# Performance work log

Measured on AMD Instinct MI355X. Metric: run time of the kernel, lower is better.

## Reference

```python
import jax, jax.numpy as jnp
import numpy as np

H = 16  # num_heads

def setup_inputs() -> dict:
    key = jax.random.key(0)
    ks = jax.random.split(key, 6)
    B, T, C, S = 2, 2048, 1024, 2048
    return {
        "q": jax.random.normal(ks[0], (B, T, C), jnp.float32),
        "k_xl": jax.random.normal(ks[1], (B, S, C), jnp.float32),
        "v_xl": jax.random.normal(ks[2], (B, S, C), jnp.float32),
        "W_qkv": jax.random.normal(ks[3], (3 * C, C), jnp.float32) * (1.0 / np.sqrt(C)),
        "W_proj": jax.random.normal(ks[4], (C, C), jnp.float32) * (1.0 / np.sqrt(C)),
        "pos_emb": jax.random.normal(ks[5], (S, C), jnp.float32),
        "is_causal": 0,
    }

def reference(q, k_xl, v_xl, W_qkv, W_proj, pos_emb, is_causal):
    B, T, C = q.shape
    hd = C // H
    # self_attention: W_qkv(q).split(d_model, -1)
    qkv = jnp.einsum('btc,dc->btd', q, W_qkv)  # [B,T,3C]
    qn, kn, vn = jnp.split(qkv, 3, axis=-1)
    # XL cache gets positional embedding added before use
    kx = k_xl + pos_emb[None, :, :]            # [B,S,C]
    vx = v_xl

    def to_heads(x):
        b, s, c = x.shape
        return x.reshape(b, s, H, hd).transpose(0, 2, 1, 3)  # [B,H,s,hd]

    qh = to_heads(qn)
    kcat = jnp.concatenate([to_heads(kx), to_heads(kn)], axis=2)  # [B,H,S+T,hd]
    vcat = jnp.concatenate([to_heads(vx), to_heads(vn)], axis=2)
    scale = 1.0 / jnp.sqrt(jnp.asarray(hd, qh.dtype))
    scores = jnp.einsum('bhtd,bhsd->bhts', qh, kcat) * scale  # [B,H,T,S+T]
    attn = jax.nn.softmax(scores, axis=-1)
    y = jnp.einsum('bhts,bhsd->bhtd', attn, vcat)  # [B,H,T,hd]
    y = y.transpose(0, 2, 1, 3).reshape(B, T, C)
    return jnp.einsum('btc,dc->btd', y, W_proj)
```

## Files before the change

kernel.cpp:

```cpp
#include <hip/hip_runtime.h>

typedef unsigned short u16;
typedef unsigned int u32;
typedef u16 u16x4 __attribute__((ext_vector_type(4)));
typedef u16 u16x8 __attribute__((ext_vector_type(8)));
typedef __bf16 bf16x8 __attribute__((ext_vector_type(8)));
typedef float f32x4 __attribute__((ext_vector_type(4)));
typedef float f32x16 __attribute__((ext_vector_type(16)));

static __device__ __forceinline__ u16 f2bf(float f) {
  union { float f; u32 u; } x; x.f = f;
  u32 r = x.u + 0x7fffu + ((x.u >> 16) & 1u);
  return (u16)(r >> 16);
}
static __device__ __forceinline__ u32 packbf(float a, float b) {
  union { u32 u; __bf16 h[2]; } x; x.h[0] = (__bf16)a; x.h[1] = (__bf16)b; return x.u;
}
static __device__ __forceinline__ void pl32swap(u32& a, u32& b) {
  asm volatile("v_permlane32_swap_b32 %0, %1" : "+v"(a), "+v"(b));
}
static __device__ __forceinline__ void gload16(const void* g, void* l) {
  __builtin_amdgcn_global_load_lds((const __attribute__((address_space(1))) unsigned int*)g,
                                   (__attribute__((address_space(3))) unsigned int*)l, 16, 0, 0);
}

__global__ __launch_bounds__(256) void cvt_all(const float* __restrict__ q, const float* __restrict__ wqkv_f,
                                               const float* __restrict__ wproj_f, u16* __restrict__ qbf,
                                               u16* __restrict__ wqkv, u16* __restrict__ wproj, float sc) {
  int i = blockIdx.x * 256 + threadIdx.x;
  const float* src;
  u16* dst;
  int j;
  float s = 1.0f;
  if (i < 1048576) { src = q; dst = qbf; j = i; }
  else if (i < 1835008) { j = i - 1048576; src = wqkv_f; dst = wqkv; if (j < 262144) s = sc; }
  else { j = i - 1835008; src = wproj_f; dst = wproj; }
  float4 v = reinterpret_cast<const float4*>(src)[j];
  u16x4 o; o[0] = f2bf(v.x * s); o[1] = f2bf(v.y * s); o[2] = f2bf(v.z * s); o[3] = f2bf(v.w * s);
  reinterpret_cast<u16x4*>(dst)[j] = o;
}

template <int OUT_BF16>
__global__ __launch_bounds__(256, 2) void gemm_bt2(const u16* __restrict__ A, const u16* __restrict__ B,
                                                   void* __restrict__ Cout, int M, int N, int K) {
  __shared__ alignas(128) u16 As[8192];
  __shared__ alignas(128) u16 Bs[8192];
  const int tid = threadIdx.x;
  const int m0 = blockIdx.y * 128, n0 = blockIdx.x * 128;
  const int wid = tid >> 6, lane = tid & 63;
  const int lm = lane & 15, lg = lane >> 4;
  const int wm = (wid >> 1) * 64, wn = (wid & 1) * 64;
  int srow[4], scol[4];
#pragma unroll
  for (int i = 0; i < 4; i++) {
    int li = tid + i * 256;
    srow[i] = li >> 3;
    scol[i] = ((li & 7) ^ (srow[i] & 7)) * 8;
  }
  f32x4 acc[4][4] = {};
  for (int k0 = 0; k0 < K; k0 += 64) {
    __syncthreads();
#pragma unroll
    for (int i = 0; i < 4; i++) {
      gload16(&A[(size_t)(m0 + srow[i]) * K + k0 + scol[i]], &As[(size_t)(i * 256 + wid * 64) * 8]);
      gload16(&B[(size_t)(n0 + srow[i]) * K + k0 + scol[i]], &Bs[(size_t)(i * 256 + wid * 64) * 8]);
    }
    __syncthreads();
#pragma unroll
    for (int ks = 0; ks < 2; ks++) {
      bf16x8 af[4], bfr[4];
#pragma unroll
      for (int mi = 0; mi < 4; mi++) {
        int row = wm + mi * 16 + lm;
        af[mi] = *(const bf16x8*)&As[row * 64 + (((ks * 4 + lg) ^ (row & 7)) << 3)];
      }
#pragma unroll
      for (int ni = 0; ni < 4; ni++) {
        int row = wn + ni * 16 + lm;
        bfr[ni] = *(const bf16x8*)&Bs[row * 64 + (((ks * 4 + lg) ^ (row & 7)) << 3)];
      }
#pragma unroll
      for (int mi = 0; mi < 4; mi++)
#pragma unroll
        for (int ni = 0; ni < 4; ni++)
          acc[mi][ni] = __builtin_amdgcn_mfma_f32_16x16x32_bf16(af[mi], bfr[ni], acc[mi][ni], 0, 0, 0);
    }
  }
#pragma unroll
  for (int mi = 0; mi < 4; mi++)
#pragma unroll
    for (int ni = 0; ni < 4; ni++)
#pragma unroll
      for (int r = 0; r < 4; r++) {
        int row = m0 + wm + mi * 16 + lg * 4 + r;
        int col = n0 + wn + ni * 16 + lm;
        if (OUT_BF16) ((u16*)Cout)[(size_t)row * N + col] = f2bf(acc[mi][ni][r]);
        else          ((float*)Cout)[(size_t)row * N + col] = acc[mi][ni][r];
      }
}

__global__ __launch_bounds__(256) void build_kxl(const float* __restrict__ k_xl, const float* __restrict__ pos,
                                                 u16* __restrict__ khxl) {
  int idx = blockIdx.x * 256 + threadIdx.x;
  int d8 = idx & 7;
  int s = (idx >> 3) & 2047;
  int bh = idx >> 14;
  int b = bh >> 4, h = bh & 15;
  size_t src = ((size_t)(b * 2048 + s)) * 1024 + h * 64 + d8 * 8;
  size_t ps = ((size_t)s) * 1024 + h * 64 + d8 * 8;
  float4 a0 = *(const float4*)&k_xl[src];
  float4 a1 = *(const float4*)&k_xl[src + 4];
  float4 p0 = *(const float4*)&pos[ps];
  float4 p1 = *(const float4*)&pos[ps + 4];
  u16x8 o;
  o[0] = f2bf(a0.x + p0.x); o[1] = f2bf(a0.y + p0.y); o[2] = f2bf(a0.z + p0.z); o[3] = f2bf(a0.w + p0.w);
  o[4] = f2bf(a1.x + p1.x); o[5] = f2bf(a1.y + p1.y); o[6] = f2bf(a1.z + p1.z); o[7] = f2bf(a1.w + p1.w);
  *(u16x8*)&khxl[((size_t)bh * 2048 + s) * 64 + d8 * 8] = o;
}

__global__ __launch_bounds__(256) void build_vt(const float* __restrict__ v_xl, const u16* __restrict__ qkvb,
                                                u16* __restrict__ Vt) {
  __shared__ u16 tile[64][72];
  const int bh = blockIdx.y, b = bh >> 4, h = bh & 15;
  const int s0 = blockIdx.x * 64;
  const int tid = threadIdx.x;
  {
    int sl = tid >> 2;
    int dseg = (tid & 3) * 16;
    if (s0 < 2048) {
      const float* src = v_xl + ((size_t)(b * 2048 + s0 + sl)) * 1024 + h * 64 + dseg;
#pragma unroll
      for (int j = 0; j < 16; j += 4) {
        float4 v = *(const float4*)&src[j];
        tile[sl][dseg + j] = f2bf(v.x);
        tile[sl][dseg + j + 1] = f2bf(v.y);
        tile[sl][dseg + j + 2] = f2bf(v.z);
        tile[sl][dseg + j + 3] = f2bf(v.w);
      }
    } else {
      const u16* src = qkvb + ((size_t)(b * 2048 + s0 - 2048 + sl)) * 3072 + 2048 + h * 64 + dseg;
      *(u16x8*)&tile[sl][dseg] = *(const u16x8*)&src[0];
      *(u16x8*)&tile[sl][dseg + 8] = *(const u16x8*)&src[8];
    }
  }
  __syncthreads();
  {
    int d = tid >> 2;
    int sseg = (tid & 3) * 16;
    u16* dst = Vt + ((size_t)bh * 64 + d) * 4096 + s0 + sseg;
    u16x8 o0, o1;
#pragma unroll
    for (int j = 0; j < 8; j++) { o0[j] = tile[sseg + j][d]; o1[j] = tile[sseg + 8 + j][d]; }
    *(u16x8*)&dst[0] = o0;
    *(u16x8*)&dst[8] = o1;
  }
}

__global__ __launch_bounds__(256, 4) void attn_fwd5(const u16* __restrict__ qkvb, const u16* __restrict__ khxl,
                                                    const u16* __restrict__ vt, u16* __restrict__ Y) {
  const int T = 2048;
  __shared__ alignas(128) u16 KsF[2][4096];
  __shared__ alignas(128) u16 VsF[2][4096];
  const int bh = blockIdx.y;
  const int q0 = blockIdx.x * 64;
  const int tid = threadIdx.x, wid = tid >> 6, lane = tid & 63;
  const int qt = wid & 1, ks = wid >> 1;
  const int l31 = lane & 31, hi = lane >> 5;
  const int sw = l31 & 7;
  const int b = bh >> 4, h = bh & 15;
  const int q = q0 + qt * 32 + l31;
  const u16* Qp = qkvb + (size_t)(b * T + q) * 3072 + h * 64;
  bf16x8 qf[4];
#pragma unroll
  for (int c = 0; c < 4; c++) qf[c] = *(const bf16x8*)&Qp[c * 16 + hi * 8];
  const u16* kxl_p[2];
  const u16* knew_p[2];
  const u16* v_p[2];
  int dsto[2];
#pragma unroll
  for (int i = 0; i < 2; i++) {
    int li = tid + i * 256;
    int srow = li >> 3, scol = ((li & 7) ^ (srow & 7)) * 8;
    kxl_p[i] = khxl + (size_t)bh * 2048 * 64 + (size_t)srow * 64 + scol;
    knew_p[i] = qkvb + (size_t)(b * T + srow) * 3072 + 1024 + h * 64 + scol;
    v_p[i] = vt + ((size_t)bh * 64 + srow) * 4096 + scol;
    dsto[i] = (i * 256 + wid * 64) * 8;
  }
  f32x16 accA = {0.0f}, accB = {0.0f};
  float lrun = 0.0f;
#pragma unroll
  for (int i = 0; i < 2; i++) {
    gload16(kxl_p[i], &KsF[0][dsto[i]]);
    gload16(v_p[i], &VsF[0][dsto[i]]);
  }
  int cur = 0;
  const int krow = ks * 32 + l31;
  for (int t = 0; t < 64; ++t) {
    __syncthreads();
    if (t + 1 < 64) {
      const int nt = t + 1;
#pragma unroll
      for (int i = 0; i < 2; i++) {
        const u16* ksrc = (nt < 32) ? kxl_p[i] + (size_t)nt * 4096
                                    : knew_p[i] + (size_t)(nt - 32) * 196608;
        gload16(ksrc, &KsF[cur ^ 1][dsto[i]]);
        gload16(v_p[i] + nt * 64, &VsF[cur ^ 1][dsto[i]]);
      }
    }
    const u16* Ksb = KsF[cur];
    const u16* Vsb = VsF[cur];
    f32x16 s = {0.0f};
    __builtin_amdgcn_s_setprio(1);
#pragma unroll
    for (int c = 0; c < 4; c++) {
      int cg = 2 * c + hi;
      bf16x8 kf = *(const bf16x8*)&Ksb[krow * 64 + ((cg ^ sw) << 3)];
      s = __builtin_amdgcn_mfma_f32_32x32x16_bf16(kf, qf[c], s, 0, 0, 0);
    }
    __builtin_amdgcn_s_setprio(0);
#pragma unroll
    for (int r = 0; r < 16; r++) s[r] = __builtin_amdgcn_exp2f(s[r]);
    float r0 = ((s[0] + s[1]) + (s[2] + s[3])) + ((s[4] + s[5]) + (s[6] + s[7]));
    float r1 = ((s[8] + s[9]) + (s[10] + s[11])) + ((s[12] + s[13]) + (s[14] + s[15]));
    lrun += r0 + r1;
    u32 w[4][2];
#pragma unroll
    for (int g = 0; g < 4; g++) {
      w[g][0] = packbf(s[4 * g + 0], s[4 * g + 1]);
      w[g][1] = packbf(s[4 * g + 2], s[4 * g + 3]);
    }
    __builtin_amdgcn_s_setprio(1);
#pragma unroll
    for (int m2 = 0; m2 < 2; m2++) {
      int m = ks * 2 + m2;
      u32 W0 = w[2 * m2][0], W2 = w[2 * m2 + 1][0];
      pl32swap(W0, W2);
      u32 W1 = w[2 * m2][1], W3 = w[2 * m2 + 1][1];
      pl32swap(W1, W3);
      union { u32 u[4]; bf16x8 v; } pf;
      pf.u[0] = W0; pf.u[1] = W1; pf.u[2] = W2; pf.u[3] = W3;
      int cg = 2 * m + hi;
      bf16x8 v0 = *(const bf16x8*)&Vsb[l31 * 64 + ((cg ^ sw) << 3)];
      bf16x8 v1 = *(const bf16x8*)&Vsb[(32 + l31) * 64 + ((cg ^ sw) << 3)];
      accA = __builtin_amdgcn_mfma_f32_32x32x16_bf16(v0, pf.v, accA, 0, 0, 0);
      accB = __builtin_amdgcn_mfma_f32_32x32x16_bf16(v1, pf.v, accB, 0, 0, 0);
    }
    __builtin_amdgcn_s_setprio(0);
    cur ^= 1;
  }
  float lt = lrun + __shfl_xor(lrun, 32);
  __syncthreads();
  float* CB = (float*)KsF;
  if (ks) {
    float* p = CB + (size_t)(qt * 64 + lane) * 33;
#pragma unroll
    for (int r = 0; r < 16; r++) { p[r] = accA[r]; p[16 + r] = accB[r]; }
    p[32] = lt;
  }
  __syncthreads();
  if (!ks) {
    const float* p = CB + (size_t)(qt * 64 + lane) * 33;
#pragma unroll
    for (int r = 0; r < 16; r++) { accA[r] += p[r]; accB[r] += p[16 + r]; }
    lt += p[32];
    float inv = 1.0f / lt;
    u16* Ts = (u16*)((char*)VsF + 1024 + qt * 4096);
#pragma unroll
    for (int dt = 0; dt < 2; dt++)
#pragma unroll
      for (int r2 = 0; r2 < 4; r2++) {
        u16x4 o;
#pragma unroll
        for (int e = 0; e < 4; e++) {
          float v = dt ? accB[4 * r2 + e] : accA[4 * r2 + e];
          o[e] = f2bf(v * inv);
        }
        int dbase = dt * 32 + r2 * 8 + hi * 4;
        int byteoff = l31 * 128 + ((dbase * 2) ^ (sw << 4));
        *(u16x4*)((char*)Ts + byteoff) = o;
      }
#pragma unroll
    for (int p4 = 0; p4 < 4; p4++) {
      int row = p4 * 8 + (lane >> 3);
      int c16 = lane & 7;
      u16x8 v = *(const u16x8*)((const char*)Ts + row * 128 + ((c16 << 4) ^ ((row & 7) << 4)));
      *(u16x8*)&Y[((size_t)(b * T + q0 + qt * 32 + row)) * 1024 + h * 64 + c16 * 8] = v;
    }
  }
}

extern "C" void kernel_launch(void* const* d_in, const int* in_sizes, int n_in,
                              void* d_out, int out_size, void* d_ws, size_t ws_size,
                              hipStream_t stream) {
  const float* q = (const float*)d_in[0];
  const float* k_xl = (const float*)d_in[1];
  const float* v_xl = (const float*)d_in[2];
  const float* W_qkv = (const float*)d_in[3];
  const float* W_proj = (const float*)d_in[4];
  const float* pos = (const float*)d_in[5];

  u16* wqkv = (u16*)d_ws;
  u16* wproj = wqkv + (size_t)3072 * 1024;
  u16* qbf = wproj + (size_t)1024 * 1024;
  u16* qkvb = qbf + (size_t)4096 * 1024;
  u16* khxl = qkvb + (size_t)4096 * 3072;
  u16* vt = khxl + (size_t)4 * 1024 * 1024;
  u16* ybf = vt + (size_t)8 * 1024 * 1024;

  const float SC = 0.125f * 1.4426950408889634f;

  cvt_all<<<8192, 256, 0, stream>>>(q, W_qkv, W_proj, qbf, wqkv, wproj, SC);

  gemm_bt2<1><<<dim3(24, 32), 256, 0, stream>>>(qbf, wqkv, qkvb, 4096, 3072, 1024);

  build_kxl<<<2048, 256, 0, stream>>>(k_xl, pos, khxl);
  build_vt<<<dim3(64, 32), 256, 0, stream>>>(v_xl, qkvb, vt);

  attn_fwd5<<<dim3(32, 32), 256, 0, stream>>>(qkvb, khxl, vt, ybf);

  gemm_bt2<0><<<dim3(8, 32), 256, 0, stream>>>(ybf, wproj, d_out, 4096, 1024, 1024);
}
```

Before: 180.3 us.

## Fuse k_xl build into conversion, double-buffer GEMMs, load K to registers in attention

The separate k_xl positional-add kernel is folded into the fp32-to-bf16 conversion launch, which removes one kernel launch. The GEMM now double-buffers its LDS tiles and prefetches the next K-slice during the MFMAs, so one barrier per iteration goes away. The attention kernel loads K fragments straight from global memory into registers, ping-ponging between two sets, and only V goes through LDS. It also uses a swizzled, vectorized cross-warp reduction. In exchange the GEMM uses twice the LDS, which may reduce occupancy, and the direct K loads may coalesce less well.

```diff
diff --git a/kernel.cpp b/kernel.cpp
--- a/kernel.cpp
+++ b/kernel.cpp
@@ -24,60 +24,90 @@
                                    (__attribute__((address_space(3))) unsigned int*)l, 16, 0, 0);
 }
 
-__global__ __launch_bounds__(256) void cvt_all(const float* __restrict__ q, const float* __restrict__ wqkv_f,
-                                               const float* __restrict__ wproj_f, u16* __restrict__ qbf,
-                                               u16* __restrict__ wqkv, u16* __restrict__ wproj, float sc) {
+__global__ __launch_bounds__(256) void cvt_fuse(const float* __restrict__ q, const float* __restrict__ wqkv_f,
+                                                const float* __restrict__ wproj_f, const float* __restrict__ k_xl,
+                                                const float* __restrict__ pos, u16* __restrict__ qbf,
+                                                u16* __restrict__ wqkv, u16* __restrict__ wproj,
+                                                u16* __restrict__ khxl, float sc) {
   int i = blockIdx.x * 256 + threadIdx.x;
-  const float* src;
-  u16* dst;
-  int j;
-  float s = 1.0f;
-  if (i < 1048576) { src = q; dst = qbf; j = i; }
-  else if (i < 1835008) { j = i - 1048576; src = wqkv_f; dst = wqkv; if (j < 262144) s = sc; }
-  else { j = i - 1835008; src = wproj_f; dst = wproj; }
-  float4 v = reinterpret_cast<const float4*>(src)[j];
-  u16x4 o; o[0] = f2bf(v.x * s); o[1] = f2bf(v.y * s); o[2] = f2bf(v.z * s); o[3] = f2bf(v.w * s);
-  reinterpret_cast<u16x4*>(dst)[j] = o;
+  if (i < 2097152) {
+    const float* src;
+    u16* dst;
+    int j;
+    float s = 1.0f;
+    if (i < 1048576) { src = q; dst = qbf; j = i; }
+    else if (i < 1835008) { j = i - 1048576; src = wqkv_f; dst = wqkv; if (j < 262144) s = sc; }
+    else { j = i - 1835008; src = wproj_f; dst = wproj; }
+    float4 v = reinterpret_cast<const float4*>(src)[j];
+    u16x4 o; o[0] = f2bf(v.x * s); o[1] = f2bf(v.y * s); o[2] = f2bf(v.z * s); o[3] = f2bf(v.w * s);
+    reinterpret_cast<u16x4*>(dst)[j] = o;
+  } else {
+    int idx = i - 2097152;
+    int d8 = idx & 7;
+    int s = (idx >> 3) & 2047;
+    int bh = idx >> 14;
+    int b = bh >> 4, h = bh & 15;
+    size_t src = ((size_t)(b * 2048 + s)) * 1024 + h * 64 + d8 * 8;
+    size_t ps = ((size_t)s) * 1024 + h * 64 + d8 * 8;
+    float4 a0 = *(const float4*)&k_xl[src];
+    float4 a1 = *(const float4*)&k_xl[src + 4];
+    float4 p0 = *(const float4*)&pos[ps];
+    float4 p1 = *(const float4*)&pos[ps + 4];
+    u16x8 o;
+    o[0] = f2bf(a0.x + p0.x); o[1] = f2bf(a0.y + p0.y); o[2] = f2bf(a0.z + p0.z); o[3] = f2bf(a0.w + p0.w);
+    o[4] = f2bf(a1.x + p1.x); o[5] = f2bf(a1.y + p1.y); o[6] = f2bf(a1.z + p1.z); o[7] = f2bf(a1.w + p1.w);
+    *(u16x8*)&khxl[((size_t)bh * 2048 + s) * 64 + d8 * 8] = o;
+  }
 }
 
 template <int OUT_BF16>
-__global__ __launch_bounds__(256, 2) void gemm_bt2(const u16* __restrict__ A, const u16* __restrict__ B,
+__global__ __launch_bounds__(256, 2) void gemm_bt3(const u16* __restrict__ A, const u16* __restrict__ B,
                                                    void* __restrict__ Cout, int M, int N, int K) {
-  __shared__ alignas(128) u16 As[8192];
-  __shared__ alignas(128) u16 Bs[8192];
+  __shared__ alignas(128) u16 As[2][8192];
+  __shared__ alignas(128) u16 Bs[2][8192];
   const int tid = threadIdx.x;
   const int m0 = blockIdx.y * 128, n0 = blockIdx.x * 128;
   const int wid = tid >> 6, lane = tid & 63;
   const int lm = lane & 15, lg = lane >> 4;
   const int wm = (wid >> 1) * 64, wn = (wid & 1) * 64;
-  int srow[4], scol[4];
+  int srow[4], scol[4], dsto[4];
 #pragma unroll
   for (int i = 0; i < 4; i++) {
     int li = tid + i * 256;
     srow[i] = li >> 3;
     scol[i] = ((li & 7) ^ (srow[i] & 7)) * 8;
+    dsto[i] = (i * 256 + wid * 64) * 8;
   }
   f32x4 acc[4][4] = {};
+#pragma unroll
+  for (int i = 0; i < 4; i++) {
+    gload16(&A[(size_t)(m0 + srow[i]) * K + scol[i]], &As[0][dsto[i]]);
+    gload16(&B[(size_t)(n0 + srow[i]) * K + scol[i]], &Bs[0][dsto[i]]);
+  }
+  int cur = 0;
   for (int k0 = 0; k0 < K; k0 += 64) {
     __syncthreads();
-#pragma unroll
-    for (int i = 0; i < 4; i++) {
-      gload16(&A[(size_t)(m0 + srow[i]) * K + k0 + scol[i]], &As[(size_t)(i * 256 + wid * 64) * 8]);
-      gload16(&B[(size_t)(n0 + srow[i]) * K + k0 + scol[i]], &Bs[(size_t)(i * 256 + wid * 64) * 8]);
-    }
-    __syncthreads();
+    if (k0 + 64 < K) {
+#pragma unroll
+      for (int i = 0; i < 4; i++) {
+        gload16(&A[(size_t)(m0 + srow[i]) * K + k0 + 64 + scol[i]], &As[cur ^ 1][dsto[i]]);
+        gload16(&B[(size_t)(n0 + srow[i]) * K + k0 + 64 + scol[i]], &Bs[cur ^ 1][dsto[i]]);
+      }
+    }
+    const u16* Asb = As[cur];
+    const u16* Bsb = Bs[cur];
 #pragma unroll
     for (int ks = 0; ks < 2; ks++) {
       bf16x8 af[4], bfr[4];
 #pragma unroll
       for (int mi = 0; mi < 4; mi++) {
         int row = wm + mi * 16 + lm;
-        af[mi] = *(const bf16x8*)&As[row * 64 + (((ks * 4 + lg) ^ (row & 7)) << 3)];
+        af[mi] = *(const bf16x8*)&Asb[row * 64 + (((ks * 4 + lg) ^ (row & 7)) << 3)];
       }
 #pragma unroll
       for (int ni = 0; ni < 4; ni++) {
         int row = wn + ni * 16 + lm;
-        bfr[ni] = *(const bf16x8*)&Bs[row * 64 + (((ks * 4 + lg) ^ (row & 7)) << 3)];
+        bfr[ni] = *(const bf16x8*)&Bsb[row * 64 + (((ks * 4 + lg) ^ (row & 7)) << 3)];
       }
 #pragma unroll
       for (int mi = 0; mi < 4; mi++)
@@ -85,6 +115,7 @@
         for (int ni = 0; ni < 4; ni++)
           acc[mi][ni] = __builtin_amdgcn_mfma_f32_16x16x32_bf16(af[mi], bfr[ni], acc[mi][ni], 0, 0, 0);
     }
+    cur ^= 1;
   }
 #pragma unroll
   for (int mi = 0; mi < 4; mi++)
@@ -97,25 +128,6 @@
         if (OUT_BF16) ((u16*)Cout)[(size_t)row * N + col] = f2bf(acc[mi][ni][r]);
         else          ((float*)Cout)[(size_t)row * N + col] = acc[mi][ni][r];
       }
-}
-
-__global__ __launch_bounds__(256) void build_kxl(const float* __restrict__ k_xl, const float* __restrict__ pos,
-                                                 u16* __restrict__ khxl) {
-  int idx = blockIdx.x * 256 + threadIdx.x;
-  int d8 = idx & 7;
-  int s = (idx >> 3) & 2047;
-  int bh = idx >> 14;
-  int b = bh >> 4, h = bh & 15;
-  size_t src = ((size_t)(b * 2048 + s)) * 1024 + h * 64 + d8 * 8;
-  size_t ps = ((size_t)s) * 1024 + h * 64 + d8 * 8;
-  float4 a0 = *(const float4*)&k_xl[src];
-  float4 a1 = *(const float4*)&k_xl[src + 4];
-  float4 p0 = *(const float4*)&pos[ps];
-  float4 p1 = *(const float4*)&pos[ps + 4];
-  u16x8 o;
-  o[0] = f2bf(a0.x + p0.x); o[1] = f2bf(a0.y + p0.y); o[2] = f2bf(a0.z + p0.z); o[3] = f2bf(a0.w + p0.w);
-  o[4] = f2bf(a1.x + p1.x); o[5] = f2bf(a1.y + p1.y); o[6] = f2bf(a1.z + p1.z); o[7] = f2bf(a1.w + p1.w);
-  *(u16x8*)&khxl[((size_t)bh * 2048 + s) * 64 + d8 * 8] = o;
 }
 
 __global__ __launch_bounds__(256) void build_vt(const float* __restrict__ v_xl, const u16* __restrict__ qkvb,
@@ -156,11 +168,58 @@
   }
 }
 
-__global__ __launch_bounds__(256, 4) void attn_fwd5(const u16* __restrict__ qkvb, const u16* __restrict__ khxl,
+#define ATTN_BODY(T, KF, KN, CUR)                                              \
+  {                                                                            \
+    __syncthreads();                                                           \
+    if ((T) + 1 < 64) {                                                        \
+      _Pragma("unroll")                                                        \
+      for (int i = 0; i < 2; i++)                                              \
+        gload16(v_p[i] + ((T) + 1) * 64, &VsF[(CUR) ^ 1][dsto[i]]);            \
+      const u16* kp = ((T) + 1 < 32) ? kxlb + (size_t)((T) + 1) * 4096         \
+                                     : knewb + (size_t)((T) + 1 - 32) * 196608;\
+      _Pragma("unroll")                                                        \
+      for (int c = 0; c < 4; c++) KN[c] = *(const bf16x8*)&kp[c * 16];         \
+    }                                                                          \
+    f32x16 s = {0.0f};                                                         \
+    __builtin_amdgcn_s_setprio(1);                                             \
+    _Pragma("unroll")                                                          \
+    for (int c = 0; c < 4; c++)                                                \
+      s = __builtin_amdgcn_mfma_f32_32x32x16_bf16(KF[c], qf[c], s, 0, 0, 0);   \
+    __builtin_amdgcn_s_setprio(0);                                             \
+    _Pragma("unroll")                                                          \
+    for (int r = 0; r < 16; r++) s[r] = __builtin_amdgcn_exp2f(s[r]);          \
+    lrun += (((s[0] + s[1]) + (s[2] + s[3])) + ((s[4] + s[5]) + (s[6] + s[7])))\
+          + (((s[8] + s[9]) + (s[10] + s[11])) + ((s[12] + s[13]) + (s[14] + s[15]))); \
+    u32 w[4][2];                                                               \
+    _Pragma("unroll")                                                          \
+    for (int g = 0; g < 4; g++) {                                              \
+      w[g][0] = packbf(s[4 * g + 0], s[4 * g + 1]);                            \
+      w[g][1] = packbf(s[4 * g + 2], s[4 * g + 3]);                            \
+    }                                                                          \
+    const u16* Vsb = VsF[(CUR)];                                               \
+    __builtin_amdgcn_s_setprio(1);                                             \
+    _Pragma("unroll")                                                          \
+    for (int m2 = 0; m2 < 2; m2++) {                                           \
+      u32 W0 = w[2 * m2][0], W2 = w[2 * m2 + 1][0];                            \
+      pl32swap(W0, W2);                                                        \
+      u32 W1 = w[2 * m2][1], W3 = w[2 * m2 + 1][1];                            \
+      pl32swap(W1, W3);                                                        \
+      union { u32 u[4]; bf16x8 v; } pf;                                        \
+      pf.u[0] = W0; pf.u[1] = W1; pf.u[2] = W2; pf.u[3] = W3;                  \
+      int cg = 2 * (ks * 2 + m2) + hi;                                         \
+      bf16x8 v0 = *(const bf16x8*)&Vsb[l31 * 64 + ((cg ^ sw) << 3)];           \
+      bf16x8 v1 = *(const bf16x8*)&Vsb[(32 + l31) * 64 + ((cg ^ sw) << 3)];    \
+      accA = __builtin_amdgcn_mfma_f32_32x32x16_bf16(v0, pf.v, accA, 0, 0, 0); \
+      accB = __builtin_amdgcn_mfma_f32_32x32x16_bf16(v1, pf.v, accB, 0, 0, 0); \
+    }                                                                          \
+    __builtin_amdgcn_s_setprio(0);                                             \
+  }
+
+__global__ __launch_bounds__(256, 4) void attn_fwd6(const u16* __restrict__ qkvb, const u16* __restrict__ khxl,
                                                     const u16* __restrict__ vt, u16* __restrict__ Y) {
   const int T = 2048;
-  __shared__ alignas(128) u16 KsF[2][4096];
   __shared__ alignas(128) u16 VsF[2][4096];
+  __shared__ float CBl[64];
   const int bh = blockIdx.y;
   const int q0 = blockIdx.x * 64;
   const int tid = threadIdx.x, wid = tid >> 6, lane = tid & 63;
@@ -173,98 +232,61 @@
   bf16x8 qf[4];
 #pragma unroll
   for (int c = 0; c < 4; c++) qf[c] = *(const bf16x8*)&Qp[c * 16 + hi * 8];
-  const u16* kxl_p[2];
-  const u16* knew_p[2];
+  const int krow0 = ks * 32 + l31;
+  const u16* kxlb = khxl + ((size_t)bh * 2048 + krow0) * 64 + hi * 8;
+  const u16* knewb = qkvb + (size_t)(b * T + krow0) * 3072 + 1024 + h * 64 + hi * 8;
   const u16* v_p[2];
   int dsto[2];
 #pragma unroll
   for (int i = 0; i < 2; i++) {
     int li = tid + i * 256;
     int srow = li >> 3, scol = ((li & 7) ^ (srow & 7)) * 8;
-    kxl_p[i] = khxl + (size_t)bh * 2048 * 64 + (size_t)srow * 64 + scol;
-    knew_p[i] = qkvb + (size_t)(b * T + srow) * 3072 + 1024 + h * 64 + scol;
     v_p[i] = vt + ((size_t)bh * 64 + srow) * 4096 + scol;
     dsto[i] = (i * 256 + wid * 64) * 8;
   }
   f32x16 accA = {0.0f}, accB = {0.0f};
   float lrun = 0.0f;
-#pragma unroll
-  for (int i = 0; i < 2; i++) {
-    gload16(kxl_p[i], &KsF[0][dsto[i]]);
-    gload16(v_p[i], &VsF[0][dsto[i]]);
-  }
-  int cur = 0;
-  const int krow = ks * 32 + l31;
-  for (int t = 0; t < 64; ++t) {
-    __syncthreads();
-    if (t + 1 < 64) {
-      const int nt = t + 1;
-#pragma unroll
-      for (int i = 0; i < 2; i++) {
-        const u16* ksrc = (nt < 32) ? kxl_p[i] + (size_t)nt * 4096
-                                    : knew_p[i] + (size_t)(nt - 32) * 196608;
-        gload16(ksrc, &KsF[cur ^ 1][dsto[i]]);
-        gload16(v_p[i] + nt * 64, &VsF[cur ^ 1][dsto[i]]);
-      }
-    }
-    const u16* Ksb = KsF[cur];
-    const u16* Vsb = VsF[cur];
-    f32x16 s = {0.0f};
-    __builtin_amdgcn_s_setprio(1);
-#pragma unroll
-    for (int c = 0; c < 4; c++) {
-      int cg = 2 * c + hi;
-      bf16x8 kf = *(const bf16x8*)&Ksb[krow * 64 + ((cg ^ sw) << 3)];
-      s = __builtin_amdgcn_mfma_f32_32x32x16_bf16(kf, qf[c], s, 0, 0, 0);
-    }
-    __builtin_amdgcn_s_setprio(0);
-#pragma unroll
-    for (int r = 0; r < 16; r++) s[r] = __builtin_amdgcn_exp2f(s[r]);
-    float r0 = ((s[0] + s[1]) + (s[2] + s[3])) + ((s[4] + s[5]) + (s[6] + s[7]));
-    float r1 = ((s[8] + s[9]) + (s[10] + s[11])) + ((s[12] + s[13]) + (s[14] + s[15]));
-    lrun += r0 + r1;
-    u32 w[4][2];
-#pragma unroll
-    for (int g = 0; g < 4; g++) {
-      w[g][0] = packbf(s[4 * g + 0], s[4 * g + 1]);
-      w[g][1] = packbf(s[4 * g + 2], s[4 * g + 3]);
-    }
-    __builtin_amdgcn_s_setprio(1);
-#pragma unroll
-    for (int m2 = 0; m2 < 2; m2++) {
-      int m = ks * 2 + m2;
-      u32 W0 = w[2 * m2][0], W2 = w[2 * m2 + 1][0];
-      pl32swap(W0, W2);
-      u32 W1 = w[2 * m2][1], W3 = w[2 * m2 + 1][1];
-      pl32swap(W1, W3);
-      union { u32 u[4]; bf16x8 v; } pf;
-      pf.u[0] = W0; pf.u[1] = W1; pf.u[2] = W2; pf.u[3] = W3;
-      int cg = 2 * m + hi;
-      bf16x8 v0 = *(const bf16x8*)&Vsb[l31 * 64 + ((cg ^ sw) << 3)];
-      bf16x8 v1 = *(const bf16x8*)&Vsb[(32 + l31) * 64 + ((cg ^ sw) << 3)];
-      accA = __builtin_amdgcn_mfma_f32_32x32x16_bf16(v0, pf.v, accA, 0, 0, 0);
-      accB = __builtin_amdgcn_mfma_f32_32x32x16_bf16(v1, pf.v, accB, 0, 0, 0);
-    }
-    __builtin_amdgcn_s_setprio(0);
-    cur ^= 1;
+  bf16x8 kA[4], kB[4];
+#pragma unroll
+  for (int i = 0; i < 2; i++) gload16(v_p[i], &VsF[0][dsto[i]]);
+#pragma unroll
+  for (int c = 0; c < 4; c++) kA[c] = *(const bf16x8*)&kxlb[c * 16];
+  for (int tp = 0; tp < 32; ++tp) {
+    ATTN_BODY(2 * tp, kA, kB, 0)
+    ATTN_BODY(2 * tp + 1, kB, kA, 1)
   }
   float lt = lrun + __shfl_xor(lrun, 32);
   __syncthreads();
-  float* CB = (float*)KsF;
+  float* CB = (float*)VsF;
   if (ks) {
-    float* p = CB + (size_t)(qt * 64 + lane) * 33;
-#pragma unroll
-    for (int r = 0; r < 16; r++) { p[r] = accA[r]; p[16 + r] = accB[r]; }
-    p[32] = lt;
+    float* p = CB + (size_t)(qt * 64 + lane) * 32;
+#pragma unroll
+    for (int j = 0; j < 8; j++) {
+      f32x4 u;
+#pragma unroll
+      for (int e = 0; e < 4; e++) u[e] = (j < 4) ? accA[4 * j + e] : accB[4 * (j - 4) + e];
+      *(f32x4*)&p[4 * (j ^ (lane & 7))] = u;
+    }
+    if (hi == 0) CBl[qt * 32 + l31] = lt;
   }
   __syncthreads();
   if (!ks) {
-    const float* p = CB + (size_t)(qt * 64 + lane) * 33;
-#pragma unroll
-    for (int r = 0; r < 16; r++) { accA[r] += p[r]; accB[r] += p[16 + r]; }
-    lt += p[32];
+    const float* p = CB + (size_t)(qt * 64 + lane) * 32;
+#pragma unroll
+    for (int j = 0; j < 8; j++) {
+      f32x4 u = *(const f32x4*)&p[4 * (j ^ (lane & 7))];
+#pragma unroll
+      for (int e = 0; e < 4; e++) {
+        if (j < 4) accA[4 * j + e] += u[e];
+        else       accB[4 * (j - 4) + e] += u[e];
+      }
+    }
+    lt += CBl[qt * 32 + l31];
+  }
+  __syncthreads();
+  if (!ks) {
     float inv = 1.0f / lt;
-    u16* Ts = (u16*)((char*)VsF + 1024 + qt * 4096);
+    u16* Ts = (u16*)VsF + qt * 2048;
 #pragma unroll
     for (int dt = 0; dt < 2; dt++)
 #pragma unroll
@@ -309,14 +331,13 @@
 
   const float SC = 0.125f * 1.4426950408889634f;
 
-  cvt_all<<<8192, 256, 0, stream>>>(q, W_qkv, W_proj, qbf, wqkv, wproj, SC);
-
-  gemm_bt2<1><<<dim3(24, 32), 256, 0, stream>>>(qbf, wqkv, qkvb, 4096, 3072, 1024);
-
-  build_kxl<<<2048, 256, 0, stream>>>(k_xl, pos, khxl);
+  cvt_fuse<<<10240, 256, 0, stream>>>(q, W_qkv, W_proj, k_xl, pos, qbf, wqkv, wproj, khxl, SC);
+
+  gemm_bt3<1><<<dim3(24, 32), 256, 0, stream>>>(qbf, wqkv, qkvb, 4096, 3072, 1024);
+
   build_vt<<<dim3(64, 32), 256, 0, stream>>>(v_xl, qkvb, vt);
 
-  attn_fwd5<<<dim3(32, 32), 256, 0, stream>>>(qkvb, khxl, vt, ybf);
-
-  gemm_bt2<0><<<dim3(8, 32), 256, 0, stream>>>(ybf, wproj, d_out, 4096, 1024, 1024);
-}
+  attn_fwd6<<<dim3(32, 32), 256, 0, stream>>>(qkvb, khxl, vt, ybf);
+
+  gemm_bt3<0><<<dim3(8, 32), 256, 0, stream>>>(ybf, wproj, d_out, 4096, 1024, 1024);
+}
```

New measurement: 225.0 us. 24.8% more time.

## Double-buffer GEMM loads, fuse kxl build, and widen attention blocks to 512 threads

Applied to the files above, without the earlier changes.

The GEMM now prefetches the next K tile into a second LDS buffer while computing the current one, removing one barrier per iteration. The k_xl+pos bf16 build is folded into the conversion kernel, saving a launch. The attention kernel uses 512-thread blocks covering 128 queries with swizzled block-to-tile mapping, so each block shares K/V tiles across more queries, and its split-K reduction uses vectorized swizzled LDS writes. The larger blocks and doubled GEMM LDS could reduce occupancy.

```diff
diff --git a/kernel.cpp b/kernel.cpp
--- a/kernel.cpp
+++ b/kernel.cpp
@@ -24,60 +24,90 @@
                                    (__attribute__((address_space(3))) unsigned int*)l, 16, 0, 0);
 }
 
-__global__ __launch_bounds__(256) void cvt_all(const float* __restrict__ q, const float* __restrict__ wqkv_f,
-                                               const float* __restrict__ wproj_f, u16* __restrict__ qbf,
-                                               u16* __restrict__ wqkv, u16* __restrict__ wproj, float sc) {
+__global__ __launch_bounds__(256) void cvt_fuse(const float* __restrict__ q, const float* __restrict__ wqkv_f,
+                                                const float* __restrict__ wproj_f, const float* __restrict__ k_xl,
+                                                const float* __restrict__ pos, u16* __restrict__ qbf,
+                                                u16* __restrict__ wqkv, u16* __restrict__ wproj,
+                                                u16* __restrict__ khxl, float sc) {
   int i = blockIdx.x * 256 + threadIdx.x;
-  const float* src;
-  u16* dst;
-  int j;
-  float s = 1.0f;
-  if (i < 1048576) { src = q; dst = qbf; j = i; }
-  else if (i < 1835008) { j = i - 1048576; src = wqkv_f; dst = wqkv; if (j < 262144) s = sc; }
-  else { j = i - 1835008; src = wproj_f; dst = wproj; }
-  float4 v = reinterpret_cast<const float4*>(src)[j];
-  u16x4 o; o[0] = f2bf(v.x * s); o[1] = f2bf(v.y * s); o[2] = f2bf(v.z * s); o[3] = f2bf(v.w * s);
-  reinterpret_cast<u16x4*>(dst)[j] = o;
+  if (i < 2097152) {
+    const float* src;
+    u16* dst;
+    int j;
+    float s = 1.0f;
+    if (i < 1048576) { src = q; dst = qbf; j = i; }
+    else if (i < 1835008) { j = i - 1048576; src = wqkv_f; dst = wqkv; if (j < 262144) s = sc; }
+    else { j = i - 1835008; src = wproj_f; dst = wproj; }
+    float4 v = reinterpret_cast<const float4*>(src)[j];
+    u16x4 o; o[0] = f2bf(v.x * s); o[1] = f2bf(v.y * s); o[2] = f2bf(v.z * s); o[3] = f2bf(v.w * s);
+    reinterpret_cast<u16x4*>(dst)[j] = o;
+  } else {
+    int idx = i - 2097152;
+    int d8 = idx & 7;
+    int s = (idx >> 3) & 2047;
+    int bh = idx >> 14;
+    int b = bh >> 4, h = bh & 15;
+    size_t src = ((size_t)(b * 2048 + s)) * 1024 + h * 64 + d8 * 8;
+    size_t ps = ((size_t)s) * 1024 + h * 64 + d8 * 8;
+    float4 a0 = *(const float4*)&k_xl[src];
+    float4 a1 = *(const float4*)&k_xl[src + 4];
+    float4 p0 = *(const float4*)&pos[ps];
+    float4 p1 = *(const float4*)&pos[ps + 4];
+    u16x8 o;
+    o[0] = f2bf(a0.x + p0.x); o[1] = f2bf(a0.y + p0.y); o[2] = f2bf(a0.z + p0.z); o[3] = f2bf(a0.w + p0.w);
+    o[4] = f2bf(a1.x + p1.x); o[5] = f2bf(a1.y + p1.y); o[6] = f2bf(a1.z + p1.z); o[7] = f2bf(a1.w + p1.w);
+    *(u16x8*)&khxl[((size_t)bh * 2048 + s) * 64 + d8 * 8] = o;
+  }
 }
 
 template <int OUT_BF16>
-__global__ __launch_bounds__(256, 2) void gemm_bt2(const u16* __restrict__ A, const u16* __restrict__ B,
+__global__ __launch_bounds__(256, 2) void gemm_bt3(const u16* __restrict__ A, const u16* __restrict__ B,
                                                    void* __restrict__ Cout, int M, int N, int K) {
-  __shared__ alignas(128) u16 As[8192];
-  __shared__ alignas(128) u16 Bs[8192];
+  __shared__ alignas(128) u16 As[2][8192];
+  __shared__ alignas(128) u16 Bs[2][8192];
   const int tid = threadIdx.x;
   const int m0 = blockIdx.y * 128, n0 = blockIdx.x * 128;
   const int wid = tid >> 6, lane = tid & 63;
   const int lm = lane & 15, lg = lane >> 4;
   const int wm = (wid >> 1) * 64, wn = (wid & 1) * 64;
-  int srow[4], scol[4];
+  int srow[4], scol[4], dsto[4];
 #pragma unroll
   for (int i = 0; i < 4; i++) {
     int li = tid + i * 256;
     srow[i] = li >> 3;
     scol[i] = ((li & 7) ^ (srow[i] & 7)) * 8;
+    dsto[i] = (i * 256 + wid * 64) * 8;
   }
   f32x4 acc[4][4] = {};
+#pragma unroll
+  for (int i = 0; i < 4; i++) {
+    gload16(&A[(size_t)(m0 + srow[i]) * K + scol[i]], &As[0][dsto[i]]);
+    gload16(&B[(size_t)(n0 + srow[i]) * K + scol[i]], &Bs[0][dsto[i]]);
+  }
+  int cur = 0;
   for (int k0 = 0; k0 < K; k0 += 64) {
     __syncthreads();
-#pragma unroll
-    for (int i = 0; i < 4; i++) {
-      gload16(&A[(size_t)(m0 + srow[i]) * K + k0 + scol[i]], &As[(size_t)(i * 256 + wid * 64) * 8]);
-      gload16(&B[(size_t)(n0 + srow[i]) * K + k0 + scol[i]], &Bs[(size_t)(i * 256 + wid * 64) * 8]);
-    }
-    __syncthreads();
+    if (k0 + 64 < K) {
+#pragma unroll
+      for (int i = 0; i < 4; i++) {
+        gload16(&A[(size_t)(m0 + srow[i]) * K + k0 + 64 + scol[i]], &As[cur ^ 1][dsto[i]]);
+        gload16(&B[(size_t)(n0 + srow[i]) * K + k0 + 64 + scol[i]], &Bs[cur ^ 1][dsto[i]]);
+      }
+    }
+    const u16* Asb = As[cur];
+    const u16* Bsb = Bs[cur];
 #pragma unroll
     for (int ks = 0; ks < 2; ks++) {
       bf16x8 af[4], bfr[4];
 #pragma unroll
       for (int mi = 0; mi < 4; mi++) {
         int row = wm + mi * 16 + lm;
-        af[mi] = *(const bf16x8*)&As[row * 64 + (((ks * 4 + lg) ^ (row & 7)) << 3)];
+        af[mi] = *(const bf16x8*)&Asb[row * 64 + (((ks * 4 + lg) ^ (row & 7)) << 3)];
       }
 #pragma unroll
       for (int ni = 0; ni < 4; ni++) {
         int row = wn + ni * 16 + lm;
-        bfr[ni] = *(const bf16x8*)&Bs[row * 64 + (((ks * 4 + lg) ^ (row & 7)) << 3)];
+        bfr[ni] = *(const bf16x8*)&Bsb[row * 64 + (((ks * 4 + lg) ^ (row & 7)) << 3)];
       }
 #pragma unroll
       for (int mi = 0; mi < 4; mi++)
@@ -85,6 +115,7 @@
         for (int ni = 0; ni < 4; ni++)
           acc[mi][ni] = __builtin_amdgcn_mfma_f32_16x16x32_bf16(af[mi], bfr[ni], acc[mi][ni], 0, 0, 0);
     }
+    cur ^= 1;
   }
 #pragma unroll
   for (int mi = 0; mi < 4; mi++)
@@ -97,25 +128,6 @@
         if (OUT_BF16) ((u16*)Cout)[(size_t)row * N + col] = f2bf(acc[mi][ni][r]);
         else          ((float*)Cout)[(size_t)row * N + col] = acc[mi][ni][r];
       }
-}
-
-__global__ __launch_bounds__(256) void build_kxl(const float* __restrict__ k_xl, const float* __restrict__ pos,
-                                                 u16* __restrict__ khxl) {
-  int idx = blockIdx.x * 256 + threadIdx.x;
-  int d8 = idx & 7;
-  int s = (idx >> 3) & 2047;
-  int bh = idx >> 14;
-  int b = bh >> 4, h = bh & 15;
-  size_t src = ((size_t)(b * 2048 + s)) * 1024 + h * 64 + d8 * 8;
-  size_t ps = ((size_t)s) * 1024 + h * 64 + d8 * 8;
-  float4 a0 = *(const float4*)&k_xl[src];
-  float4 a1 = *(const float4*)&k_xl[src + 4];
-  float4 p0 = *(const float4*)&pos[ps];
-  float4 p1 = *(const float4*)&pos[ps + 4];
-  u16x8 o;
-  o[0] = f2bf(a0.x + p0.x); o[1] = f2bf(a0.y + p0.y); o[2] = f2bf(a0.z + p0.z); o[3] = f2bf(a0.w + p0.w);
-  o[4] = f2bf(a1.x + p1.x); o[5] = f2bf(a1.y + p1.y); o[6] = f2bf(a1.z + p1.z); o[7] = f2bf(a1.w + p1.w);
-  *(u16x8*)&khxl[((size_t)bh * 2048 + s) * 64 + d8 * 8] = o;
 }
 
 __global__ __launch_bounds__(256) void build_vt(const float* __restrict__ v_xl, const u16* __restrict__ qkvb,
@@ -156,15 +168,17 @@
   }
 }
 
-__global__ __launch_bounds__(256, 4) void attn_fwd5(const u16* __restrict__ qkvb, const u16* __restrict__ khxl,
+__global__ __launch_bounds__(512, 4) void attn_fwd7(const u16* __restrict__ qkvb, const u16* __restrict__ khxl,
                                                     const u16* __restrict__ vt, u16* __restrict__ Y) {
   const int T = 2048;
-  __shared__ alignas(128) u16 KsF[2][4096];
-  __shared__ alignas(128) u16 VsF[2][4096];
-  const int bh = blockIdx.y;
-  const int q0 = blockIdx.x * 64;
+  __shared__ alignas(128) u16 lds[16384];
+  __shared__ float CBl[128];
+  const int dd = blockIdx.x + (blockIdx.y << 4);
+  const int w = ((dd & 7) << 6) + (dd >> 3);
+  const int bh = w >> 4;
+  const int q0 = (w & 15) * 128;
   const int tid = threadIdx.x, wid = tid >> 6, lane = tid & 63;
-  const int qt = wid & 1, ks = wid >> 1;
+  const int qt = wid >> 1, ks = wid & 1;
   const int l31 = lane & 31, hi = lane >> 5;
   const int sw = l31 & 7;
   const int b = bh >> 4, h = bh & 15;
@@ -173,42 +187,28 @@
   bf16x8 qf[4];
 #pragma unroll
   for (int c = 0; c < 4; c++) qf[c] = *(const bf16x8*)&Qp[c * 16 + hi * 8];
-  const u16* kxl_p[2];
-  const u16* knew_p[2];
-  const u16* v_p[2];
-  int dsto[2];
-#pragma unroll
-  for (int i = 0; i < 2; i++) {
-    int li = tid + i * 256;
-    int srow = li >> 3, scol = ((li & 7) ^ (srow & 7)) * 8;
-    kxl_p[i] = khxl + (size_t)bh * 2048 * 64 + (size_t)srow * 64 + scol;
-    knew_p[i] = qkvb + (size_t)(b * T + srow) * 3072 + 1024 + h * 64 + scol;
-    v_p[i] = vt + ((size_t)bh * 64 + srow) * 4096 + scol;
-    dsto[i] = (i * 256 + wid * 64) * 8;
-  }
+  const int srow = tid >> 3, scol = ((tid & 7) ^ (srow & 7)) * 8;
+  const u16* kxl_p = khxl + ((size_t)bh * 2048 + srow) * 64 + scol;
+  const u16* knew_p = qkvb + (size_t)(b * T + srow) * 3072 + 1024 + h * 64 + scol;
+  const u16* v_p = vt + ((size_t)bh * 64 + srow) * 4096 + scol;
+  const int dsto = tid * 8;
   f32x16 accA = {0.0f}, accB = {0.0f};
   float lrun = 0.0f;
-#pragma unroll
-  for (int i = 0; i < 2; i++) {
-    gload16(kxl_p[i], &KsF[0][dsto[i]]);
-    gload16(v_p[i], &VsF[0][dsto[i]]);
-  }
+  gload16(kxl_p, &lds[dsto]);
+  gload16(v_p, &lds[8192 + dsto]);
   int cur = 0;
   const int krow = ks * 32 + l31;
   for (int t = 0; t < 64; ++t) {
     __syncthreads();
     if (t + 1 < 64) {
       const int nt = t + 1;
-#pragma unroll
-      for (int i = 0; i < 2; i++) {
-        const u16* ksrc = (nt < 32) ? kxl_p[i] + (size_t)nt * 4096
-                                    : knew_p[i] + (size_t)(nt - 32) * 196608;
-        gload16(ksrc, &KsF[cur ^ 1][dsto[i]]);
-        gload16(v_p[i] + nt * 64, &VsF[cur ^ 1][dsto[i]]);
-      }
-    }
-    const u16* Ksb = KsF[cur];
-    const u16* Vsb = VsF[cur];
+      const u16* ksrc = (nt < 32) ? kxl_p + (size_t)nt * 4096
+                                  : knew_p + (size_t)(nt - 32) * 196608;
+      gload16(ksrc, &lds[(cur ^ 1) * 4096 + dsto]);
+      gload16(v_p + nt * 64, &lds[8192 + (cur ^ 1) * 4096 + dsto]);
+    }
+    const u16* Ksb = &lds[cur * 4096];
+    const u16* Vsb = &lds[8192 + cur * 4096];
     f32x16 s = {0.0f};
     __builtin_amdgcn_s_setprio(1);
 #pragma unroll
@@ -223,19 +223,19 @@
     float r0 = ((s[0] + s[1]) + (s[2] + s[3])) + ((s[4] + s[5]) + (s[6] + s[7]));
     float r1 = ((s[8] + s[9]) + (s[10] + s[11])) + ((s[12] + s[13]) + (s[14] + s[15]));
     lrun += r0 + r1;
-    u32 w[4][2];
+    u32 w4[4][2];
 #pragma unroll
     for (int g = 0; g < 4; g++) {
-      w[g][0] = packbf(s[4 * g + 0], s[4 * g + 1]);
-      w[g][1] = packbf(s[4 * g + 2], s[4 * g + 3]);
+      w4[g][0] = packbf(s[4 * g + 0], s[4 * g + 1]);
+      w4[g][1] = packbf(s[4 * g + 2], s[4 * g + 3]);
     }
     __builtin_amdgcn_s_setprio(1);
 #pragma unroll
     for (int m2 = 0; m2 < 2; m2++) {
       int m = ks * 2 + m2;
-      u32 W0 = w[2 * m2][0], W2 = w[2 * m2 + 1][0];
+      u32 W0 = w4[2 * m2][0], W2 = w4[2 * m2 + 1][0];
       pl32swap(W0, W2);
-      u32 W1 = w[2 * m2][1], W3 = w[2 * m2 + 1][1];
+      u32 W1 = w4[2 * m2][1], W3 = w4[2 * m2 + 1][1];
       pl32swap(W1, W3);
       union { u32 u[4]; bf16x8 v; } pf;
       pf.u[0] = W0; pf.u[1] = W1; pf.u[2] = W2; pf.u[3] = W3;
@@ -250,21 +250,33 @@
   }
   float lt = lrun + __shfl_xor(lrun, 32);
   __syncthreads();
-  float* CB = (float*)KsF;
+  float* CB = (float*)lds;
   if (ks) {
-    float* p = CB + (size_t)(qt * 64 + lane) * 33;
-#pragma unroll
-    for (int r = 0; r < 16; r++) { p[r] = accA[r]; p[16 + r] = accB[r]; }
-    p[32] = lt;
+    float* p = CB + (size_t)(qt * 64 + lane) * 32;
+#pragma unroll
+    for (int j = 0; j < 8; j++) {
+      f32x4 u;
+#pragma unroll
+      for (int e = 0; e < 4; e++) u[e] = (j < 4) ? accA[4 * j + e] : accB[4 * (j - 4) + e];
+      *(f32x4*)&p[4 * (j ^ (lane & 7))] = u;
+    }
+    if (hi == 0) CBl[qt * 32 + l31] = lt;
   }
   __syncthreads();
   if (!ks) {
-    const float* p = CB + (size_t)(qt * 64 + lane) * 33;
-#pragma unroll
-    for (int r = 0; r < 16; r++) { accA[r] += p[r]; accB[r] += p[16 + r]; }
-    lt += p[32];
+    const float* p = CB + (size_t)(qt * 64 + lane) * 32;
+#pragma unroll
+    for (int j = 0; j < 8; j++) {
+      f32x4 u = *(const f32x4*)&p[4 * (j ^ (lane & 7))];
+#pragma unroll
+      for (int e = 0; e < 4; e++) {
+        if (j < 4) accA[4 * j + e] += u[e];
+        else       accB[4 * (j - 4) + e] += u[e];
+      }
+    }
+    lt += CBl[qt * 32 + l31];
     float inv = 1.0f / lt;
-    u16* Ts = (u16*)((char*)VsF + 1024 + qt * 4096);
+    u16* Ts = (u16*)((char*)lds + qt * 8192);
 #pragma unroll
     for (int dt = 0; dt < 2; dt++)
 #pragma unroll
@@ -309,14 +321,13 @@
 
   const float SC = 0.125f * 1.4426950408889634f;
 
-  cvt_all<<<8192, 256, 0, stream>>>(q, W_qkv, W_proj, qbf, wqkv, wproj, SC);
-
-  gemm_bt2<1><<<dim3(24, 32), 256, 0, stream>>>(qbf, wqkv, qkvb, 4096, 3072, 1024);
-
-  build_kxl<<<2048, 256, 0, stream>>>(k_xl, pos, khxl);
+  cvt_fuse<<<10240, 256, 0, stream>>>(q, W_qkv, W_proj, k_xl, pos, qbf, wqkv, wproj, khxl, SC);
+
+  gemm_bt3<1><<<dim3(24, 32), 256, 0, stream>>>(qbf, wqkv, qkvb, 4096, 3072, 1024);
+
   build_vt<<<dim3(64, 32), 256, 0, stream>>>(v_xl, qkvb, vt);
 
-  attn_fwd5<<<dim3(32, 32), 256, 0, stream>>>(qkvb, khxl, vt, ybf);
-
-  gemm_bt2<0><<<dim3(8, 32), 256, 0, stream>>>(ybf, wproj, d_out, 4096, 1024, 1024);
-}
+  attn_fwd7<<<dim3(16, 32), 512, 0, stream>>>(qkvb, khxl, vt, ybf);
+
+  gemm_bt3<0><<<dim3(8, 32), 256, 0, stream>>>(ybf, wproj, d_out, 4096, 1024, 1024);
+}
```

Measured after the change: 173.6 us. 3.7% less time.
